# Performance work log

Measured on AMD Instinct MI355X. Metric: run time of the kernel, lower is better.

The kernel has to match this reference:

```python
import jax, jax.numpy as jnp
import numpy as np
from jax import lax


def setup_inputs() -> dict:
    key = jax.random.key(0)
    k1, k2 = jax.random.split(key)
    B, H, W, C = 32, 128, 128, 128
    KH, KW = 7, 7
    inputs = jax.random.normal(k1, (B, H, W, C), dtype=jnp.float32)
    kernels = jax.random.normal(k2, (B, KH, KW, C), dtype=jnp.float32)
    return {"inputs": inputs, "kernels": kernels}


def reference(inputs, kernels):
    # inputs: [B,H,W,C], kernels: [B,kh,kw,C] -- per-sample depthwise conv,
    # stride 1, SAME padding (TF tf.nn.depthwise_conv2d semantics = cross-correlation).
    # Fuse the per-sample batch loop into ONE grouped conv with B*C groups.
    B, H, W, C = inputs.shape
    kh, kw = kernels.shape[1], kernels.shape[2]
    # [B,H,W,C] -> [1, B*C, H, W]
    x = jnp.transpose(inputs, (0, 3, 1, 2)).reshape(1, B * C, H, W)
    # [B,kh,kw,C] -> OIHW [B*C, 1, kh, kw]; group i = (sample b, channel c)
    k = jnp.transpose(kernels, (0, 3, 1, 2)).reshape(B * C, 1, kh, kw)
    out = lax.conv_general_dilated(
        x, k,
        window_strides=(1, 1),
        padding="SAME",
        feature_group_count=B * C,
        dimension_numbers=("NCHW", "OIHW", "NCHW"),
    )
    # [1, B*C, H, W] -> [B,H,W,C]
    return jnp.transpose(out.reshape(B, C, H, W), (0, 2, 3, 1))
```

## Files before the change

### kernel.cpp

```cpp
#include <hip/hip_runtime.h>


#define BB 32
#define HH 128
#define WW 128
#define CC 128
#define KH 7
#define KW 7

#define XPT 4
#define NTAP (XPT + KW - 1)
#define XG 8
#define SLABW (XG * XPT)
#define NXS (WW / SLABW)
#define YSPLIT 4
#define YROWS (HH / YSPLIT)
#define GRID (BB * NXS * YSPLIT)
#define WSLOTS 28
#define NPASS (YROWS + KH - 1)

typedef _Float16 half2_t __attribute__((ext_vector_type(2)));

static __device__ __forceinline__ half2_t pk(float a, float b) {
#if __has_builtin(__builtin_amdgcn_cvt_pkrtz)
    return __builtin_bit_cast(half2_t, __builtin_amdgcn_cvt_pkrtz(a, b));
#else
    half2_t r; r.x = (_Float16)a; r.y = (_Float16)b; return r;
#endif
}

static __device__ __forceinline__ float dot2f(unsigned w, half2_t t, float c) {
#if __has_builtin(__builtin_amdgcn_fdot2)
    return __builtin_amdgcn_fdot2(__builtin_bit_cast(half2_t, w), t, c, false);
#else
    half2_t wv = __builtin_bit_cast(half2_t, w);
    return fmaf((float)wv.x, (float)t.x, fmaf((float)wv.y, (float)t.y, c));
#endif
}

__global__ __launch_bounds__(1024) void crossconv_kernel(
    const float* __restrict__ in,
    const float* __restrict__ ker,
    float* __restrict__ out)
{
    __shared__ unsigned lds_w[CC * WSLOTS];

    const int tid = threadIdx.x;
    const int c  = tid & (CC - 1);
    const int xg = __builtin_amdgcn_readfirstlane(tid >> 7);

    const int bid = blockIdx.x;
    const int swz = (bid & 7) * (GRID / 8) + (bid >> 3);
    const int b  = swz >> 4;
    const int xs = (swz >> 2) & 3;
    const int yh = swz & 3;
    const int x0 = xs * SLABW + xg * XPT;
    const int y0 = yh * YROWS;

    {
        const float* kb = ker + ((size_t)b * KH * KW) * CC + c;
        for (int s = xg; s < WSLOTS; s += XG) {
            const int i = s >> 2, q = s & 3;
            half2_t pr;
            if (q < 3) {
                const int f0 = i * KW + 2 * q;
                pr = pk(kb[f0 * CC], kb[(f0 + 1) * CC]);
            } else {
                pr = pk(kb[(i * KW + 6) * CC], 0.0f);
            }
            lds_w[c * WSLOTS + s] = __builtin_bit_cast(unsigned, pr);
        }
    }
    __syncthreads();

    const float* ib = in  + ((size_t)b * HH * WW) * CC;
    float*       ob = out + ((size_t)b * HH * WW) * CC;
    const unsigned* wlds = &lds_w[c * WSLOTS];

    const bool interior = (x0 >= 3) && (x0 + XPT + 2 < WW);

    auto load_taps = [&](float* t, int yi) {
        if (yi < 0 || yi >= HH) {
            #pragma unroll
            for (int j = 0; j < NTAP; ++j) t[j] = 0.0f;
            return;
        }
        const float* row = ib + (size_t)yi * WW * CC + c;
        if (interior) {
            #pragma unroll
            for (int j = 0; j < NTAP; ++j)
                t[j] = row[(x0 - 3 + j) * CC];
        } else {
            #pragma unroll
            for (int j = 0; j < NTAP; ++j) {
                const int xx = x0 - 3 + j;
                t[j] = (xx >= 0 && xx < WW) ? row[xx * CC] : 0.0f;
            }
        }
    };

    float acc[KH][XPT];
    #pragma unroll
    for (int s = 0; s < KH; ++s)
        #pragma unroll
        for (int xo = 0; xo < XPT; ++xo) acc[s][xo] = 0.0f;

    const int yi0 = y0 - 3;

    float t[NTAP];
    half2_t e[5], o[5];
    load_taps(t, yi0);
    #pragma unroll
    for (int k = 0; k < 5; ++k) e[k] = pk(t[2 * k], t[2 * k + 1]);
    #pragma unroll
    for (int k = 0; k < 4; ++k) o[k] = pk(t[2 * k + 1], t[2 * k + 2]);
    o[4] = pk(t[9], 0.0f);

    #pragma unroll 1
    for (int p = 0; p < NPASS; ++p) {
        const int yi = yi0 + p;

        load_taps(t, (p + 1 < NPASS) ? (yi + 1) : -1);

        asm volatile("" ::: "memory");

        #pragma unroll
        for (int i = 0; i < KH; ++i) {
            const uint4 wq = *(const uint4*)(wlds + i * 4);
            const int s = 6 - i;
            #pragma unroll
            for (int xo = 0; xo < XPT; ++xo) {
                float a = acc[s][xo];
                if ((xo & 1) == 0) {
                    const int k0 = xo >> 1;
                    a = dot2f(wq.x, e[k0],     a);
                    a = dot2f(wq.y, e[k0 + 1], a);
                    a = dot2f(wq.z, e[k0 + 2], a);
                    a = dot2f(wq.w, e[k0 + 3], a);
                } else {
                    const int k0 = (xo - 1) >> 1;
                    a = dot2f(wq.x, o[k0],     a);
                    a = dot2f(wq.y, o[k0 + 1], a);
                    a = dot2f(wq.z, o[k0 + 2], a);
                    a = dot2f(wq.w, o[k0 + 3], a);
                }
                acc[s][xo] = a;
            }
        }

        const int y = yi - 3;
        if (y >= y0) {
            float* orow = ob + ((size_t)y * WW + x0) * CC + c;
            #pragma unroll
            for (int xo = 0; xo < XPT; ++xo)
                orow[xo * CC] = acc[0][xo];
        }

        #pragma unroll
        for (int s = 0; s < KH - 1; ++s)
            #pragma unroll
            for (int xo = 0; xo < XPT; ++xo) acc[s][xo] = acc[s + 1][xo];
        #pragma unroll
        for (int xo = 0; xo < XPT; ++xo) acc[KH - 1][xo] = 0.0f;

        #pragma unroll
        for (int k = 0; k < 5; ++k) e[k] = pk(t[2 * k], t[2 * k + 1]);
        #pragma unroll
        for (int k = 0; k < 4; ++k) o[k] = pk(t[2 * k + 1], t[2 * k + 2]);
        o[4] = pk(t[9], 0.0f);
    }
}

extern "C" void kernel_launch(void* const* d_in, const int* in_sizes, int n_in,
                              void* d_out, int out_size, void* d_ws, size_t ws_size,
                              hipStream_t stream) {
    const float* in  = (const float*)d_in[0];
    const float* ker = (const float*)d_in[1];
    float*       out = (float*)d_out;

    crossconv_kernel<<<GRID, 1024, 0, stream>>>(in, ker, out);
}
```

Before: 143.4 us.

## Process two input rows per pass to share weight loads across rows

The row loop now handles two consecutive input rows per iteration, with an extra accumulator slot. Each weight quad read from LDS feeds the dot products of both rows, so there are half as many LDS reads and loop iterations, and more independent work for latency hiding. In exchange it drops the previous software prefetch of the next row, so both row loads now happen inside the same iteration. It also raises register pressure at 1024 threads per block.

```diff
diff --git a/kernel.cpp b/kernel.cpp
--- a/kernel.cpp
+++ b/kernel.cpp
@@ -17,7 +17,7 @@
 #define YROWS (HH / YSPLIT)
 #define GRID (BB * NXS * YSPLIT)
 #define WSLOTS 28
-#define NPASS (YROWS + KH - 1)
+#define NPASS ((YROWS + KH - 1) / 2)
 
 typedef _Float16 half2_t __attribute__((ext_vector_type(2)));
 
@@ -99,75 +99,94 @@
         }
     };
 
-    float acc[KH][XPT];
+    float acc[KH + 1][XPT];
     #pragma unroll
-    for (int s = 0; s < KH; ++s)
+    for (int s = 0; s < KH + 1; ++s)
         #pragma unroll
         for (int xo = 0; xo < XPT; ++xo) acc[s][xo] = 0.0f;
 
     const int yi0 = y0 - 3;
-
-    float t[NTAP];
-    half2_t e[5], o[5];
-    load_taps(t, yi0);
-    #pragma unroll
-    for (int k = 0; k < 5; ++k) e[k] = pk(t[2 * k], t[2 * k + 1]);
-    #pragma unroll
-    for (int k = 0; k < 4; ++k) o[k] = pk(t[2 * k + 1], t[2 * k + 2]);
-    o[4] = pk(t[9], 0.0f);
 
     #pragma unroll 1
     for (int p = 0; p < NPASS; ++p) {
-        const int yi = yi0 + p;
-
-        load_taps(t, (p + 1 < NPASS) ? (yi + 1) : -1);
+        const int yi = yi0 + 2 * p;
+
+        float ta[NTAP], tb[NTAP];
+        load_taps(ta, yi);
+        load_taps(tb, yi + 1);
+
+        half2_t eA[5], oA[5], eB[5], oB[5];
+        #pragma unroll
+        for (int k = 0; k < 5; ++k) eA[k] = pk(ta[2 * k], ta[2 * k + 1]);
+        #pragma unroll
+        for (int k = 0; k < 4; ++k) oA[k] = pk(ta[2 * k + 1], ta[2 * k + 2]);
+        oA[4] = pk(ta[9], 0.0f);
+        #pragma unroll
+        for (int k = 0; k < 5; ++k) eB[k] = pk(tb[2 * k], tb[2 * k + 1]);
+        #pragma unroll
+        for (int k = 0; k < 4; ++k) oB[k] = pk(tb[2 * k + 1], tb[2 * k + 2]);
+        oB[4] = pk(tb[9], 0.0f);
 
         asm volatile("" ::: "memory");
 
         #pragma unroll
         for (int i = 0; i < KH; ++i) {
             const uint4 wq = *(const uint4*)(wlds + i * 4);
-            const int s = 6 - i;
             #pragma unroll
             for (int xo = 0; xo < XPT; ++xo) {
-                float a = acc[s][xo];
+                float a = acc[6 - i][xo];
+                float a2 = acc[7 - i][xo];
                 if ((xo & 1) == 0) {
                     const int k0 = xo >> 1;
-                    a = dot2f(wq.x, e[k0],     a);
-                    a = dot2f(wq.y, e[k0 + 1], a);
-                    a = dot2f(wq.z, e[k0 + 2], a);
-                    a = dot2f(wq.w, e[k0 + 3], a);
+                    a  = dot2f(wq.x, eA[k0],     a);
+                    a  = dot2f(wq.y, eA[k0 + 1], a);
+                    a  = dot2f(wq.z, eA[k0 + 2], a);
+                    a  = dot2f(wq.w, eA[k0 + 3], a);
+                    a2 = dot2f(wq.x, eB[k0],     a2);
+                    a2 = dot2f(wq.y, eB[k0 + 1], a2);
+                    a2 = dot2f(wq.z, eB[k0 + 2], a2);
+                    a2 = dot2f(wq.w, eB[k0 + 3], a2);
                 } else {
                     const int k0 = (xo - 1) >> 1;
-                    a = dot2f(wq.x, o[k0],     a);
-                    a = dot2f(wq.y, o[k0 + 1], a);
-                    a = dot2f(wq.z, o[k0 + 2], a);
-                    a = dot2f(wq.w, o[k0 + 3], a);
+                    a  = dot2f(wq.x, oA[k0],     a);
+                    a  = dot2f(wq.y, oA[k0 + 1], a);
+                    a  = dot2f(wq.z, oA[k0 + 2], a);
+                    a  = dot2f(wq.w, oA[k0 + 3], a);
+                    a2 = dot2f(wq.x, oB[k0],     a2);
+                    a2 = dot2f(wq.y, oB[k0 + 1], a2);
+                    a2 = dot2f(wq.z, oB[k0 + 2], a2);
+                    a2 = dot2f(wq.w, oB[k0 + 3], a2);
                 }
-                acc[s][xo] = a;
-            }
-        }
-
-        const int y = yi - 3;
-        if (y >= y0) {
-            float* orow = ob + ((size_t)y * WW + x0) * CC + c;
-            #pragma unroll
-            for (int xo = 0; xo < XPT; ++xo)
-                orow[xo * CC] = acc[0][xo];
+                acc[6 - i][xo] = a;
+                acc[7 - i][xo] = a2;
+            }
+        }
+
+        {
+            const int y = yi - 3;
+            if (y >= y0) {
+                float* orow = ob + ((size_t)y * WW + x0) * CC + c;
+                #pragma unroll
+                for (int xo = 0; xo < XPT; ++xo)
+                    orow[xo * CC] = acc[0][xo];
+            }
+            if (y + 1 >= y0) {
+                float* orow = ob + ((size_t)(y + 1) * WW + x0) * CC + c;
+                #pragma unroll
+                for (int xo = 0; xo < XPT; ++xo)
+                    orow[xo * CC] = acc[1][xo];
+            }
         }
 
         #pragma unroll
         for (int s = 0; s < KH - 1; ++s)
             #pragma unroll
-            for (int xo = 0; xo < XPT; ++xo) acc[s][xo] = acc[s + 1][xo];
-        #pragma unroll
-        for (int xo = 0; xo < XPT; ++xo) acc[KH - 1][xo] = 0.0f;
-
-        #pragma unroll
-        for (int k = 0; k < 5; ++k) e[k] = pk(t[2 * k], t[2 * k + 1]);
-        #pragma unroll
-        for (int k = 0; k < 4; ++k) o[k] = pk(t[2 * k + 1], t[2 * k + 2]);
-        o[4] = pk(t[9], 0.0f);
+            for (int xo = 0; xo < XPT; ++xo) acc[s][xo] = acc[s + 2][xo];
+        #pragma unroll
+        for (int xo = 0; xo < XPT; ++xo) {
+            acc[KH - 1][xo] = 0.0f;
+            acc[KH][xo]     = 0.0f;
+        }
     }
 }
 
```

Result: no change. 142.9 us (-0.3%).

## Stage input rows through double-buffered LDS with vectorized float4 loads

Applied to the files above, without the earlier changes.

Each input row slab (40 columns x 128 channels) is now loaded once per block with coalesced float4 global loads into a double-buffered LDS area, and threads read their 10 taps from LDS. Before, each thread did 10 scalar global loads, and neighbouring x-groups fetched overlapping halo columns redundantly. The prefetch of the next row is held in registers and written to LDS after compute. The cost is a __syncthreads every row pass and about 40KB more LDS per block, which can lower occupancy.

```diff
diff --git a/kernel.cpp b/kernel.cpp
--- a/kernel.cpp
+++ b/kernel.cpp
@@ -12,12 +12,14 @@
 #define NTAP (XPT + KW - 1)
 #define XG 8
 #define SLABW (XG * XPT)
+#define SLABC 40
 #define NXS (WW / SLABW)
 #define YSPLIT 4
 #define YROWS (HH / YSPLIT)
 #define GRID (BB * NXS * YSPLIT)
 #define WSLOTS 28
 #define NPASS (YROWS + KH - 1)
+#define ROWELEM (SLABC * CC)
 
 typedef _Float16 half2_t __attribute__((ext_vector_type(2)));
 
@@ -44,6 +46,7 @@
     float* __restrict__ out)
 {
     __shared__ unsigned lds_w[CC * WSLOTS];
+    __shared__ float    lds_in[2][ROWELEM];
 
     const int tid = threadIdx.x;
     const int c  = tid & (CC - 1);
@@ -54,7 +57,8 @@
     const int b  = swz >> 4;
     const int xs = (swz >> 2) & 3;
     const int yh = swz & 3;
-    const int x0 = xs * SLABW + xg * XPT;
+    const int xstart = xs * SLABW;
+    const int x0 = xstart + xg * XPT;
     const int y0 = yh * YROWS;
 
     {
@@ -71,33 +75,33 @@
             lds_w[c * WSLOTS + s] = __builtin_bit_cast(unsigned, pr);
         }
     }
+
+    const char*  inb  = (const char*)in + (size_t)b * HH * WW * CC * 4;
+    float*       ob   = out + ((size_t)b * HH * WW) * CC;
+    const unsigned* wlds = &lds_w[c * WSLOTS];
+
+    const int  coff  = (tid & 31) * 16;
+    const int  gc0   = min(max(xstart - 3 + (tid >> 5), 0), WW - 1);
+    const bool extra = (tid < 256);
+    const int  gc1   = min(max(xstart - 3 + 32 + (tid >> 5), 0), WW - 1);
+    const int  goff0 = gc0 * (CC * 4) + coff;
+    const int  goff1 = gc1 * (CC * 4) + coff;
+    const int  loff0 = tid * 16;
+    const int  loff1 = (tid + 1024) * 16;
+
+    const bool interior = (x0 >= 3) && (x0 + XPT + 2 < WW);
+    const int  yi0v = y0 - 3;
+
+    if (yi0v >= 0 && yi0v < HH) {
+        const char* rowb = inb + (size_t)yi0v * (WW * CC * 4);
+        float4 s0 = *(const float4*)(rowb + goff0);
+        *(float4*)((char*)lds_in[0] + loff0) = s0;
+        if (extra) {
+            float4 s1 = *(const float4*)(rowb + goff1);
+            *(float4*)((char*)lds_in[0] + loff1) = s1;
+        }
+    }
     __syncthreads();
-
-    const float* ib = in  + ((size_t)b * HH * WW) * CC;
-    float*       ob = out + ((size_t)b * HH * WW) * CC;
-    const unsigned* wlds = &lds_w[c * WSLOTS];
-
-    const bool interior = (x0 >= 3) && (x0 + XPT + 2 < WW);
-
-    auto load_taps = [&](float* t, int yi) {
-        if (yi < 0 || yi >= HH) {
-            #pragma unroll
-            for (int j = 0; j < NTAP; ++j) t[j] = 0.0f;
-            return;
-        }
-        const float* row = ib + (size_t)yi * WW * CC + c;
-        if (interior) {
-            #pragma unroll
-            for (int j = 0; j < NTAP; ++j)
-                t[j] = row[(x0 - 3 + j) * CC];
-        } else {
-            #pragma unroll
-            for (int j = 0; j < NTAP; ++j) {
-                const int xx = x0 - 3 + j;
-                t[j] = (xx >= 0 && xx < WW) ? row[xx * CC] : 0.0f;
-            }
-        }
-    };
 
     float acc[KH][XPT];
     #pragma unroll
@@ -105,46 +109,66 @@
         #pragma unroll
         for (int xo = 0; xo < XPT; ++xo) acc[s][xo] = 0.0f;
 
-    const int yi0 = y0 - 3;
-
-    float t[NTAP];
-    half2_t e[5], o[5];
-    load_taps(t, yi0);
-    #pragma unroll
-    for (int k = 0; k < 5; ++k) e[k] = pk(t[2 * k], t[2 * k + 1]);
-    #pragma unroll
-    for (int k = 0; k < 4; ++k) o[k] = pk(t[2 * k + 1], t[2 * k + 2]);
-    o[4] = pk(t[9], 0.0f);
-
     #pragma unroll 1
     for (int p = 0; p < NPASS; ++p) {
-        const int yi = yi0 + p;
-
-        load_taps(t, (p + 1 < NPASS) ? (yi + 1) : -1);
-
-        asm volatile("" ::: "memory");
-
-        #pragma unroll
-        for (int i = 0; i < KH; ++i) {
-            const uint4 wq = *(const uint4*)(wlds + i * 4);
-            const int s = 6 - i;
-            #pragma unroll
-            for (int xo = 0; xo < XPT; ++xo) {
-                float a = acc[s][xo];
-                if ((xo & 1) == 0) {
-                    const int k0 = xo >> 1;
-                    a = dot2f(wq.x, e[k0],     a);
-                    a = dot2f(wq.y, e[k0 + 1], a);
-                    a = dot2f(wq.z, e[k0 + 2], a);
-                    a = dot2f(wq.w, e[k0 + 3], a);
-                } else {
-                    const int k0 = (xo - 1) >> 1;
-                    a = dot2f(wq.x, o[k0],     a);
-                    a = dot2f(wq.y, o[k0 + 1], a);
-                    a = dot2f(wq.z, o[k0 + 2], a);
-                    a = dot2f(wq.w, o[k0 + 3], a);
+        const int yi = yi0v + p;
+
+        float4 g0, g1;
+        const int rnext = yi + 1;
+        const bool dostage = (rnext >= 0) && (rnext < HH) && (p + 1 < NPASS);
+        if (dostage) {
+            const char* rowb = inb + (size_t)rnext * (WW * CC * 4);
+            g0 = *(const float4*)(rowb + goff0);
+            if (extra) g1 = *(const float4*)(rowb + goff1);
+        }
+
+        if (yi >= 0 && yi < HH) {
+            const float* buf = lds_in[p & 1];
+            float t[NTAP];
+            if (interior) {
+                #pragma unroll
+                for (int j = 0; j < NTAP; ++j)
+                    t[j] = buf[(xg * XPT + j) * CC + c];
+            } else {
+                #pragma unroll
+                for (int j = 0; j < NTAP; ++j) {
+                    const int xx = x0 - 3 + j;
+                    t[j] = (xx >= 0 && xx < WW) ? buf[(xg * XPT + j) * CC + c]
+                                                : 0.0f;
                 }
-                acc[s][xo] = a;
+            }
+
+            half2_t e[5], o[5];
+            #pragma unroll
+            for (int k = 0; k < 5; ++k) e[k] = pk(t[2 * k], t[2 * k + 1]);
+            #pragma unroll
+            for (int k = 0; k < 4; ++k) o[k] = pk(t[2 * k + 1], t[2 * k + 2]);
+            o[4] = pk(t[9], 0.0f);
+
+            asm volatile("" ::: "memory");
+
+            #pragma unroll
+            for (int i = 0; i < KH; ++i) {
+                const uint4 wq = *(const uint4*)(wlds + i * 4);
+                const int s = 6 - i;
+                #pragma unroll
+                for (int xo = 0; xo < XPT; ++xo) {
+                    float a = acc[s][xo];
+                    if ((xo & 1) == 0) {
+                        const int k0 = xo >> 1;
+                        a = dot2f(wq.x, e[k0],     a);
+                        a = dot2f(wq.y, e[k0 + 1], a);
+                        a = dot2f(wq.z, e[k0 + 2], a);
+                        a = dot2f(wq.w, e[k0 + 3], a);
+                    } else {
+                        const int k0 = (xo - 1) >> 1;
+                        a = dot2f(wq.x, o[k0],     a);
+                        a = dot2f(wq.y, o[k0 + 1], a);
+                        a = dot2f(wq.z, o[k0 + 2], a);
+                        a = dot2f(wq.w, o[k0 + 3], a);
+                    }
+                    acc[s][xo] = a;
+                }
             }
         }
 
@@ -155,7 +179,6 @@
             for (int xo = 0; xo < XPT; ++xo)
                 orow[xo * CC] = acc[0][xo];
         }
-
         #pragma unroll
         for (int s = 0; s < KH - 1; ++s)
             #pragma unroll
@@ -163,11 +186,12 @@
         #pragma unroll
         for (int xo = 0; xo < XPT; ++xo) acc[KH - 1][xo] = 0.0f;
 
-        #pragma unroll
-        for (int k = 0; k < 5; ++k) e[k] = pk(t[2 * k], t[2 * k + 1]);
-        #pragma unroll
-        for (int k = 0; k < 4; ++k) o[k] = pk(t[2 * k + 1], t[2 * k + 2]);
-        o[4] = pk(t[9], 0.0f);
+        if (dostage) {
+            char* dst = (char*)lds_in[(p + 1) & 1];
+            *(float4*)(dst + loff0) = g0;
+            if (extra) *(float4*)(dst + loff1) = g1;
+        }
+        __syncthreads();
     }
 }
 
```

New measurement: 145.5 us. Within noise of the previous version (+1.5%).
